# Kernel optimization log

Measured on AMD Instinct MI355X. Metric: run time of the kernel, lower is better.

Reference implementation:

```python
import jax, jax.numpy as jnp
import numpy as np
import math

HIDDEN = 1024

def setup_inputs() -> dict:
    key = jax.random.key(0)
    k1, k2, k3, k4, k5 = jax.random.split(key, 5)
    s = 1.0 / math.sqrt(HIDDEN)
    return {
        "x": jax.random.normal(k1, (4, 2048, HIDDEN), dtype=jnp.float32),
        "W_qkv": jax.random.uniform(k2, (HIDDEN, 3 * HIDDEN), jnp.float32, -s, s),
        "b_qkv": jax.random.uniform(k3, (3 * HIDDEN,), jnp.float32, -s, s),
        "W_out": jax.random.uniform(k4, (HIDDEN, HIDDEN), jnp.float32, -s, s),
        "b_out": jax.random.uniform(k5, (HIDDEN,), jnp.float32, -s, s),
    }

def reference(x, W_qkv, b_qkv, W_out, b_out):
    # fused QKV projection: [b, s, 3h]
    qkv = jnp.einsum("bsh,hd->bsd", x, W_qkv) + b_qkv
    q, k, v = jnp.split(qkv, 3, axis=-1)
    scale = 1.0 / math.sqrt(x.shape[-1])
    scores = jnp.einsum("bqh,bkh->bqk", q, k) * scale  # [b, s, s]
    attn = jax.nn.softmax(scores, axis=-1)
    out = jnp.einsum("bqk,bkh->bqh", attn, v)
    return jnp.einsum("bsh,hd->bsd", out, W_out) + b_out
```

## Files before the change

kernel.cpp:

```cpp
#include <hip/hip_runtime.h>
#include <cstdint>
#include <cstddef>


typedef __bf16 bf16;
typedef __bf16 bf16x8 __attribute__((ext_vector_type(8)));
typedef __bf16 bf16x4 __attribute__((ext_vector_type(4)));
typedef float  f32x4  __attribute__((ext_vector_type(4)));

#define THREADS 512
#define BM 256
#define BN 256
#define UNIT 8192

__device__ __forceinline__ void gload_lds16(const bf16* g, bf16* l) {
  __builtin_amdgcn_global_load_lds(
      (const __attribute__((address_space(1))) unsigned int*)g,
      (__attribute__((address_space(3))) unsigned int*)l, 16, 0, 0);
}

__device__ __forceinline__ void stage_unit(const bf16* g0, long ld, bf16* ldsu, int tid) {
  const int wv = tid >> 6;
  #pragma unroll
  for (int j = 0; j < 2; ++j) {
    const int c = j * 512 + tid;
    const int r = c >> 3;
    const int sg = (c & 7) ^ (r & 7);
    const int cb = j * 512 + (wv << 6);
    gload_lds16(g0 + (long)r * ld + sg * 8, ldsu + (size_t)cb * 8);
  }
}

__device__ __forceinline__ bf16x8 rd_frag(const bf16* unitb, int r, int s) {
  return *(const bf16x8*)(unitb + (size_t)r * 64 + (size_t)((s ^ (r & 7)) * 8));
}

#define GATE(N)  asm volatile("s_waitcnt vmcnt(" #N ")" ::: "memory")
#define LGKM0()  asm volatile("s_waitcnt lgkmcnt(0)" ::: "memory")
#define SBAR()   __builtin_amdgcn_s_barrier()
#define SCHED0() __builtin_amdgcn_sched_barrier(0)

#define PHASE(DB, MH, NH, RA, RB, STAGE_CODE, GATE_CODE)                         \
  {                                                                              \
    if (RA) {                                                                    \
      _Pragma("unroll") for (int mf = 0; mf < 4; ++mf)                           \
        _Pragma("unroll") for (int ks = 0; ks < 2; ++ks)                         \
          aF[mf][ks] = rd_frag(&lds[DB][MH][0], wsm * 64 + mf * 16 + lr, ks * 4 + lh); \
    }                                                                            \
    if (RB) {                                                                    \
      _Pragma("unroll") for (int nf = 0; nf < 2; ++nf)                           \
        _Pragma("unroll") for (int ks = 0; ks < 2; ++ks)                         \
          bF[NH][nf][ks] = rd_frag(&lds[DB][2 + NH][0], wsn * 32 + nf * 16 + lr, ks * 4 + lh); \
    }                                                                            \
    STAGE_CODE;                                                                  \
    SBAR();                                                                      \
    LGKM0();                                                                     \
    SCHED0();                                                                    \
    __builtin_amdgcn_s_setprio(1);                                               \
    _Pragma("unroll") for (int mf = 0; mf < 4; ++mf)                             \
      _Pragma("unroll") for (int nf = 0; nf < 2; ++nf)                           \
        _Pragma("unroll") for (int ks = 0; ks < 2; ++ks)                         \
          acc[(MH)*4 + mf][(NH)*2 + nf] = __builtin_amdgcn_mfma_f32_16x16x32_bf16( \
              aF[mf][ks], bF[NH][nf][ks], acc[(MH)*4 + mf][(NH)*2 + nf], 0, 0, 0); \
    __builtin_amdgcn_s_setprio(0);                                               \
    GATE_CODE;                                                                   \
    SBAR();                                                                      \
    SCHED0();                                                                    \
  }

template <int MODE>
__device__ __forceinline__ void gemm_body(
    const bf16* __restrict__ A, long sAz, int lda,
    const bf16* __restrict__ B, long sBz, int ldb, int K,
    bf16* __restrict__ p0, long sCz, bf16* __restrict__ p1, bf16* __restrict__ p2,
    float* __restrict__ fout, const float* __restrict__ bias, float scale) {
  __shared__ bf16 lds[2][4][UNIT];
  const int tid = threadIdx.x;
  const int wv = tid >> 6, ln = tid & 63;
  const int wsm = wv >> 2, wsn = wv & 3;
  const int lr = ln & 15, lh = ln >> 4;

  const int gx = gridDim.x, gy = gridDim.y;
  const int lin = blockIdx.x + gx * (blockIdx.y + gy * blockIdx.z);
  const int nwg = gx * gy * gridDim.z;
  const int swz = (lin & 7) * (nwg >> 3) + (lin >> 3);
  const int bx = swz % gx;
  const int tq = swz / gx;
  const int by = tq % gy;
  const int z  = tq / gy;

  const int m0 = bx * BM, n0 = by * BN;
  const bf16* Ag = A + (long)z * sAz + (long)m0 * lda;
  const bf16* Bg = B + (long)z * sBz + (long)n0 * ldb;
  const int NITER = K / 128;

  stage_unit(Ag,             lda, &lds[0][0][0], tid);
  stage_unit(Bg,             ldb, &lds[0][2][0], tid);
  stage_unit(Ag + 128 * lda, lda, &lds[0][1][0], tid);
  stage_unit(Bg + 128 * ldb, ldb, &lds[0][3][0], tid);
  stage_unit(Ag + 64,        lda, &lds[1][0][0], tid);
  stage_unit(Bg + 64,        ldb, &lds[1][2][0], tid);
  GATE(8);
  SBAR();
  SCHED0();

  f32x4 acc[8][4];
  #pragma unroll
  for (int i = 0; i < 8; ++i)
    #pragma unroll
    for (int j = 0; j < 4; ++j) acc[i][j] = f32x4{0.f, 0.f, 0.f, 0.f};
  bf16x8 aF[4][2], bF[2][2][2];

  for (int it = 0; it < NITER; ++it) {
    const bool nl = (it + 1 < NITER);
    const long ktA = 2L * it + 1, ktB = 2L * it + 2, ktC = 2L * it + 3;
    PHASE(0, 0, 0, 1, 1,
      { stage_unit(Ag + 128 * lda + ktA * 64, lda, &lds[1][1][0], tid); },
      { GATE(6); });
    PHASE(0, 0, 1, 0, 1,
      { stage_unit(Bg + 128 * ldb + ktA * 64, ldb, &lds[1][3][0], tid); },
      { GATE(10); });
    PHASE(0, 1, 0, 1, 0,
      { if (nl) stage_unit(Ag + ktB * 64, lda, &lds[0][0][0], tid); },
      {});
    PHASE(0, 1, 1, 0, 0,
      { if (nl) stage_unit(Bg + ktB * 64, ldb, &lds[0][2][0], tid); },
      { if (nl) { GATE(8); } else { GATE(4); } });
    PHASE(1, 0, 0, 1, 1,
      { if (nl) stage_unit(Ag + 128 * lda + ktB * 64, lda, &lds[0][1][0], tid); },
      { if (nl) { GATE(6); } else { GATE(0); } });
    PHASE(1, 0, 1, 0, 1,
      { if (nl) stage_unit(Bg + 128 * ldb + ktB * 64, ldb, &lds[0][3][0], tid); },
      { GATE(10); });
    PHASE(1, 1, 0, 1, 0,
      { if (nl) stage_unit(Ag + ktC * 64, lda, &lds[1][0][0], tid); },
      {});
    PHASE(1, 1, 1, 0, 0,
      { if (nl) stage_unit(Bg + ktC * 64, ldb, &lds[1][2][0], tid); },
      { GATE(8); });
  }

  #pragma unroll
  for (int mi = 0; mi < 8; ++mi) {
    #pragma unroll
    for (int ni = 0; ni < 4; ++ni) {
      #pragma unroll
      for (int rg = 0; rg < 4; ++rg) {
        const int gm = m0 + (mi >> 2) * 128 + wsm * 64 + (mi & 3) * 16 + lh * 4 + rg;
        const int gn = n0 + (ni >> 1) * 128 + wsn * 32 + (ni & 1) * 16 + lr;
        float v = acc[mi][ni][rg];
        if constexpr (MODE == 0) {
          v += bias[gn];
          if (gn < 1024)       p0[(size_t)gm * 1024 + gn] = (bf16)v;
          else if (gn < 2048)  p1[(size_t)gm * 1024 + (gn - 1024)] = (bf16)v;
          else                 p2[(size_t)gm * 1024 + (gn - 2048)] = (bf16)v;
        } else if constexpr (MODE == 1) {
          p0[(size_t)z * sCz + (size_t)gm * 2048 + gn] = (bf16)(v * scale);
        } else if constexpr (MODE == 2) {
          p0[(size_t)z * sCz + (size_t)gm * 1024 + gn] = (bf16)v;
        } else {
          fout[(size_t)gm * 1024 + gn] = v + bias[gn];
        }
      }
    }
  }
}

#define GEMM_ARGS const bf16* A, long sAz, int lda, const bf16* B, long sBz, int ldb, \
                  int K, bf16* p0, long sCz, bf16* p1, bf16* p2, float* fout,         \
                  const float* bias, float scale
__global__ __launch_bounds__(THREADS, 2) void gemm_qkv(GEMM_ARGS) {
  gemm_body<0>(A, sAz, lda, B, sBz, ldb, K, p0, sCz, p1, p2, fout, bias, scale);
}
__global__ __launch_bounds__(THREADS, 2) void gemm_sc(GEMM_ARGS) {
  gemm_body<1>(A, sAz, lda, B, sBz, ldb, K, p0, sCz, p1, p2, fout, bias, scale);
}
__global__ __launch_bounds__(THREADS, 2) void gemm_pv(GEMM_ARGS) {
  gemm_body<2>(A, sAz, lda, B, sBz, ldb, K, p0, sCz, p1, p2, fout, bias, scale);
}
__global__ __launch_bounds__(THREADS, 2) void gemm_out(GEMM_ARGS) {
  gemm_body<3>(A, sAz, lda, B, sBz, ldb, K, p0, sCz, p1, p2, fout, bias, scale);
}

__global__ __launch_bounds__(256) void k_f32_to_bf16(const float* __restrict__ in,
                                                     bf16* __restrict__ out, long n) {
  long i = ((long)blockIdx.x * blockDim.x + threadIdx.x) * 4;
  if (i + 3 < n) {
    float4 v = *(const float4*)(in + i);
    bf16x4 o;
    o[0] = (bf16)v.x; o[1] = (bf16)v.y; o[2] = (bf16)v.z; o[3] = (bf16)v.w;
    *(bf16x4*)(out + i) = o;
  }
}

__global__ __launch_bounds__(256) void k_transpose(const float* __restrict__ in,
                                                   bf16* __restrict__ out, int R, int C) {
  __shared__ float t[32][33];
  int c0 = blockIdx.x * 32, r0 = blockIdx.y * 32;
  int tx = threadIdx.x, ty = threadIdx.y;
  #pragma unroll
  for (int dy = 0; dy < 32; dy += 8)
    t[ty + dy][tx] = in[(size_t)(r0 + ty + dy) * C + c0 + tx];
  __syncthreads();
  #pragma unroll
  for (int dy = 0; dy < 32; dy += 8)
    out[(size_t)(c0 + ty + dy) * R + r0 + tx] = (bf16)t[tx][ty + dy];
}

__global__ __launch_bounds__(256) void k_transpose_v(const bf16* __restrict__ in,
                                                     bf16* __restrict__ out) {
  __shared__ bf16 t[32][33];
  const int z = blockIdx.z;
  in  += (size_t)z * 2048 * 1024;
  out += (size_t)z * 1024 * 2048;
  int h0 = blockIdx.x * 32, s0 = blockIdx.y * 32;
  int tx = threadIdx.x, ty = threadIdx.y;
  #pragma unroll
  for (int dy = 0; dy < 32; dy += 8)
    t[ty + dy][tx] = in[(size_t)(s0 + ty + dy) * 1024 + h0 + tx];
  __syncthreads();
  #pragma unroll
  for (int dy = 0; dy < 32; dy += 8)
    out[(size_t)(h0 + ty + dy) * 2048 + s0 + tx] = t[tx][ty + dy];
}

__global__ __launch_bounds__(256) void k_softmax(bf16* __restrict__ S) {
  const int row = blockIdx.x;
  bf16* p = S + (size_t)row * 2048;
  const int tid = threadIdx.x;
  bf16x8 vin = *(const bf16x8*)(p + tid * 8);
  float x[8];
  float mx = -1e30f;
  #pragma unroll
  for (int i = 0; i < 8; ++i) { x[i] = (float)vin[i]; mx = fmaxf(mx, x[i]); }
  #pragma unroll
  for (int off = 32; off; off >>= 1) mx = fmaxf(mx, __shfl_down(mx, off));
  __shared__ float redm[4];
  if ((tid & 63) == 0) redm[tid >> 6] = mx;
  __syncthreads();
  mx = fmaxf(fmaxf(redm[0], redm[1]), fmaxf(redm[2], redm[3]));
  float s = 0.f;
  #pragma unroll
  for (int i = 0; i < 8; ++i) { x[i] = __expf(x[i] - mx); s += x[i]; }
  #pragma unroll
  for (int off = 32; off; off >>= 1) s += __shfl_down(s, off);
  __shared__ float reds[4];
  if ((tid & 63) == 0) reds[tid >> 6] = s;
  __syncthreads();
  s = reds[0] + reds[1] + reds[2] + reds[3];
  float inv = 1.0f / s;
  bf16x8 vo;
  #pragma unroll
  for (int i = 0; i < 8; ++i) vo[i] = (bf16)(x[i] * inv);
  *(bf16x8*)(p + tid * 8) = vo;
}

extern "C" void kernel_launch(void* const* d_in, const int* in_sizes, int n_in,
                              void* d_out, int out_size, void* d_ws, size_t ws_size,
                              hipStream_t stream) {
  const float* x    = (const float*)d_in[0];
  const float* Wqkv = (const float*)d_in[1];
  const float* bqkv = (const float*)d_in[2];
  const float* Wout = (const float*)d_in[3];
  const float* bout = (const float*)d_in[4];
  float* out = (float*)d_out;

  char* w = (char*)d_ws;
  const size_t MB = 1ull << 20;
  bf16* Xb  = (bf16*)(w);
  bf16* WqT = (bf16*)(w + 16 * MB);
  bf16* WoT = (bf16*)(w + 22 * MB);
  bf16* Qb  = (bf16*)(w + 24 * MB);
  bf16* Kb  = (bf16*)(w + 40 * MB);
  bf16* Vb  = (bf16*)(w + 56 * MB);
  bf16* Sb  = (bf16*)(w + 72 * MB);
  bf16* AO  = (bf16*)(w + 104 * MB);
  bf16* VT  = Xb;

  k_f32_to_bf16<<<8192, 256, 0, stream>>>(x, Xb, 8388608L);
  dim3 tb(32, 8);
  k_transpose<<<dim3(96, 32), tb, 0, stream>>>(Wqkv, WqT, 1024, 3072);
  k_transpose<<<dim3(32, 32), tb, 0, stream>>>(Wout, WoT, 1024, 1024);

  gemm_qkv<<<dim3(32, 12), THREADS, 0, stream>>>(
      Xb, 0L, 1024, WqT, 0L, 1024, 1024, Qb, 0L, Kb, Vb, nullptr, bqkv, 1.0f);

  k_transpose_v<<<dim3(32, 64, 4), tb, 0, stream>>>(Vb, VT);

  gemm_sc<<<dim3(8, 8, 4), THREADS, 0, stream>>>(
      Qb, 2048L * 1024, 1024, Kb, 2048L * 1024, 1024, 1024,
      Sb, 2048L * 2048, nullptr, nullptr, nullptr, nullptr, 0.03125f);

  k_softmax<<<8192, 256, 0, stream>>>(Sb);

  gemm_pv<<<dim3(8, 4, 4), THREADS, 0, stream>>>(
      Sb, 2048L * 2048, 2048, VT, 1024L * 2048, 2048, 2048,
      AO, 2048L * 1024, nullptr, nullptr, nullptr, nullptr, 1.0f);

  gemm_out<<<dim3(32, 4), THREADS, 0, stream>>>(
      AO, 0L, 1024, WoT, 0L, 1024, 1024,
      nullptr, 0L, nullptr, nullptr, out, bout, 1.0f);
}
```

Before: 245.7 us.

## Add 256x128 triple-buffered GEMM for QKV, PV and output projections

New measurement: 217.4 us. -11.5%, faster.

```diff
diff --git a/kernel.cpp b/kernel.cpp
--- a/kernel.cpp
+++ b/kernel.cpp
@@ -9,8 +9,6 @@
 typedef float  f32x4  __attribute__((ext_vector_type(4)));
 
 #define THREADS 512
-#define BM 256
-#define BN 256
 #define UNIT 8192
 
 __device__ __forceinline__ void gload_lds16(const bf16* g, bf16* l) {
@@ -39,6 +37,155 @@
 #define LGKM0()  asm volatile("s_waitcnt lgkmcnt(0)" ::: "memory")
 #define SBAR()   __builtin_amdgcn_s_barrier()
 #define SCHED0() __builtin_amdgcn_sched_barrier(0)
+
+#define BM2 256
+#define BN2 128
+#define BK2 64
+#define BUFELS (3*UNIT)
+
+template <int MODE>
+__device__ __forceinline__ void gemm2_body(
+    const bf16* __restrict__ A, long sAz, int lda,
+    const bf16* __restrict__ B, long sBz, int ldb, int K,
+    bf16* __restrict__ p0, long sCz, bf16* __restrict__ p1, bf16* __restrict__ p2,
+    float* __restrict__ fout, const float* __restrict__ bias, float scale) {
+  __shared__ bf16 lds[3 * BUFELS];
+  const int tid = threadIdx.x;
+  const int wv = tid >> 6, ln = tid & 63;
+  const int wr = wv >> 1, wc = wv & 1;
+  const int lr = ln & 15, lh = ln >> 4;
+  const int m0 = blockIdx.x * BM2, n0 = blockIdx.y * BN2;
+  const int z = blockIdx.z;
+  A += (long)z * sAz;
+  B += (long)z * sBz;
+  const bf16* Ag = A + (long)m0 * lda;
+  const bf16* Bg = B + (long)n0 * ldb;
+  const int NT = K / BK2;
+
+  #pragma unroll
+  for (int t = 0; t < 2; ++t) {
+    bf16* bb = lds + t * BUFELS;
+    stage_unit(Ag + t * BK2, lda, bb, tid);
+    stage_unit(Ag + (long)128 * lda + t * BK2, lda, bb + UNIT, tid);
+    stage_unit(Bg + t * BK2, ldb, bb + 2 * UNIT, tid);
+  }
+  GATE(6);
+  SCHED0();
+  SBAR();
+
+  f32x4 acc[4][4];
+  #pragma unroll
+  for (int i = 0; i < 4; ++i)
+    #pragma unroll
+    for (int j = 0; j < 4; ++j)
+      acc[i][j] = f32x4{0.f, 0.f, 0.f, 0.f};
+
+  const int aru = (wr & 1) * 64;
+  const int au  = wr >> 1;
+
+  int buf = 0, nb = 2;
+  for (int t = 0; t < NT; ++t) {
+    const bf16* Au = lds + buf * BUFELS + au * UNIT;
+    const bf16* Bu = lds + buf * BUFELS + 2 * UNIT;
+    bf16* Pn = lds + nb * BUFELS;
+    const bool pf = (t + 2 < NT);
+    bf16x8 aF[2][2], bF[4][2];
+
+    #pragma unroll
+    for (int i = 0; i < 2; ++i)
+      #pragma unroll
+      for (int ks = 0; ks < 2; ++ks)
+        aF[i][ks] = rd_frag(Au, aru + i * 16 + lr, (ks << 2) + lh);
+    #pragma unroll
+    for (int nf = 0; nf < 4; ++nf)
+      #pragma unroll
+      for (int ks = 0; ks < 2; ++ks)
+        bF[nf][ks] = rd_frag(Bu, wc * 64 + nf * 16 + lr, (ks << 2) + lh);
+    if (pf) {
+      stage_unit(Ag + (long)(t + 2) * BK2, lda, Pn, tid);
+      stage_unit(Ag + (long)128 * lda + (long)(t + 2) * BK2, lda, Pn + UNIT, tid);
+    }
+    SBAR();
+    LGKM0();
+    SCHED0();
+    __builtin_amdgcn_s_setprio(1);
+    #pragma unroll
+    for (int i = 0; i < 2; ++i)
+      #pragma unroll
+      for (int nf = 0; nf < 4; ++nf)
+        #pragma unroll
+        for (int ks = 0; ks < 2; ++ks)
+          acc[i][nf] = __builtin_amdgcn_mfma_f32_16x16x32_bf16(aF[i][ks], bF[nf][ks], acc[i][nf], 0, 0, 0);
+    __builtin_amdgcn_s_setprio(0);
+    SBAR();
+
+    #pragma unroll
+    for (int i = 0; i < 2; ++i)
+      #pragma unroll
+      for (int ks = 0; ks < 2; ++ks)
+        aF[i][ks] = rd_frag(Au, aru + 32 + i * 16 + lr, (ks << 2) + lh);
+    if (pf) stage_unit(Bg + (long)(t + 2) * BK2, ldb, Pn + 2 * UNIT, tid);
+    SBAR();
+    LGKM0();
+    SCHED0();
+    __builtin_amdgcn_s_setprio(1);
+    #pragma unroll
+    for (int i = 0; i < 2; ++i)
+      #pragma unroll
+      for (int nf = 0; nf < 4; ++nf)
+        #pragma unroll
+        for (int ks = 0; ks < 2; ++ks)
+          acc[2 + i][nf] = __builtin_amdgcn_mfma_f32_16x16x32_bf16(aF[i][ks], bF[nf][ks], acc[2 + i][nf], 0, 0, 0);
+    __builtin_amdgcn_s_setprio(0);
+    if (t + 1 < NT) {
+      if (pf) { GATE(6); } else { GATE(0); }
+      SCHED0();
+    }
+    SBAR();
+
+    buf = (buf == 2) ? 0 : buf + 1;
+    nb  = (nb == 2) ? 0 : nb + 1;
+  }
+
+  #pragma unroll
+  for (int mf = 0; mf < 4; ++mf) {
+    #pragma unroll
+    for (int nf = 0; nf < 4; ++nf) {
+      #pragma unroll
+      for (int rg = 0; rg < 4; ++rg) {
+        const int gm = m0 + wr * 64 + mf * 16 + lh * 4 + rg;
+        const int gn = n0 + wc * 64 + nf * 16 + lr;
+        float v = acc[mf][nf][rg];
+        if constexpr (MODE == 0) {
+          v += bias[gn];
+          if (gn < 1024)       p0[(size_t)gm * 1024 + gn] = (bf16)v;
+          else if (gn < 2048)  p1[(size_t)gm * 1024 + (gn - 1024)] = (bf16)v;
+          else                 p2[(size_t)gm * 1024 + (gn - 2048)] = (bf16)v;
+        } else if constexpr (MODE == 2) {
+          p0[(size_t)z * sCz + (size_t)gm * 1024 + gn] = (bf16)v;
+        } else {
+          fout[(size_t)gm * 1024 + gn] = v + bias[gn];
+        }
+      }
+    }
+  }
+}
+
+#define GEMM_ARGS const bf16* A, long sAz, int lda, const bf16* B, long sBz, int ldb, \
+                  int K, bf16* p0, long sCz, bf16* p1, bf16* p2, float* fout,         \
+                  const float* bias, float scale
+__global__ __launch_bounds__(THREADS, 2) void gemm_qkv(GEMM_ARGS) {
+  gemm2_body<0>(A, sAz, lda, B, sBz, ldb, K, p0, sCz, p1, p2, fout, bias, scale);
+}
+__global__ __launch_bounds__(THREADS, 2) void gemm_pv(GEMM_ARGS) {
+  gemm2_body<2>(A, sAz, lda, B, sBz, ldb, K, p0, sCz, p1, p2, fout, bias, scale);
+}
+__global__ __launch_bounds__(THREADS, 2) void gemm_out(GEMM_ARGS) {
+  gemm2_body<3>(A, sAz, lda, B, sBz, ldb, K, p0, sCz, p1, p2, fout, bias, scale);
+}
+
+#define BM8 256
+#define BN8 256
 
 #define PHASE(DB, MH, NH, RA, RB, STAGE_CODE, GATE_CODE)                         \
   {                                                                              \
@@ -68,12 +215,10 @@
     SCHED0();                                                                    \
   }
 
-template <int MODE>
-__device__ __forceinline__ void gemm_body(
+__global__ __launch_bounds__(THREADS, 2) void gemm_sc(
     const bf16* __restrict__ A, long sAz, int lda,
     const bf16* __restrict__ B, long sBz, int ldb, int K,
-    bf16* __restrict__ p0, long sCz, bf16* __restrict__ p1, bf16* __restrict__ p2,
-    float* __restrict__ fout, const float* __restrict__ bias, float scale) {
+    bf16* __restrict__ p0, long sCz, float scale) {
   __shared__ bf16 lds[2][4][UNIT];
   const int tid = threadIdx.x;
   const int wv = tid >> 6, ln = tid & 63;
@@ -84,12 +229,12 @@
   const int lin = blockIdx.x + gx * (blockIdx.y + gy * blockIdx.z);
   const int nwg = gx * gy * gridDim.z;
   const int swz = (lin & 7) * (nwg >> 3) + (lin >> 3);
-  const int bx = swz % gx;
-  const int tq = swz / gx;
-  const int by = tq % gy;
-  const int z  = tq / gy;
-
-  const int m0 = bx * BM, n0 = by * BN;
+  const int by = swz % gy;
+  const int t2 = swz / gy;
+  const int bx = t2 % gx;
+  const int z  = t2 / gx;
+
+  const int m0 = bx * BM8, n0 = by * BN8;
   const bf16* Ag = A + (long)z * sAz + (long)m0 * lda;
   const bf16* Bg = B + (long)z * sBz + (long)n0 * ldb;
   const int NITER = K / 128;
@@ -148,38 +293,10 @@
       for (int rg = 0; rg < 4; ++rg) {
         const int gm = m0 + (mi >> 2) * 128 + wsm * 64 + (mi & 3) * 16 + lh * 4 + rg;
         const int gn = n0 + (ni >> 1) * 128 + wsn * 32 + (ni & 1) * 16 + lr;
-        float v = acc[mi][ni][rg];
-        if constexpr (MODE == 0) {
-          v += bias[gn];
-          if (gn < 1024)       p0[(size_t)gm * 1024 + gn] = (bf16)v;
-          else if (gn < 2048)  p1[(size_t)gm * 1024 + (gn - 1024)] = (bf16)v;
-          else                 p2[(size_t)gm * 1024 + (gn - 2048)] = (bf16)v;
-        } else if constexpr (MODE == 1) {
-          p0[(size_t)z * sCz + (size_t)gm * 2048 + gn] = (bf16)(v * scale);
-        } else if constexpr (MODE == 2) {
-          p0[(size_t)z * sCz + (size_t)gm * 1024 + gn] = (bf16)v;
-        } else {
-          fout[(size_t)gm * 1024 + gn] = v + bias[gn];
-        }
+        p0[(size_t)z * sCz + (size_t)gm * 2048 + gn] = (bf16)(acc[mi][ni][rg] * scale);
       }
     }
   }
-}
-
-#define GEMM_ARGS const bf16* A, long sAz, int lda, const bf16* B, long sBz, int ldb, \
-                  int K, bf16* p0, long sCz, bf16* p1, bf16* p2, float* fout,         \
-                  const float* bias, float scale
-__global__ __launch_bounds__(THREADS, 2) void gemm_qkv(GEMM_ARGS) {
-  gemm_body<0>(A, sAz, lda, B, sBz, ldb, K, p0, sCz, p1, p2, fout, bias, scale);
-}
-__global__ __launch_bounds__(THREADS, 2) void gemm_sc(GEMM_ARGS) {
-  gemm_body<1>(A, sAz, lda, B, sBz, ldb, K, p0, sCz, p1, p2, fout, bias, scale);
-}
-__global__ __launch_bounds__(THREADS, 2) void gemm_pv(GEMM_ARGS) {
-  gemm_body<2>(A, sAz, lda, B, sBz, ldb, K, p0, sCz, p1, p2, fout, bias, scale);
-}
-__global__ __launch_bounds__(THREADS, 2) void gemm_out(GEMM_ARGS) {
-  gemm_body<3>(A, sAz, lda, B, sBz, ldb, K, p0, sCz, p1, p2, fout, bias, scale);
 }
 
 __global__ __launch_bounds__(256) void k_f32_to_bf16(const float* __restrict__ in,
@@ -209,18 +326,18 @@
 
 __global__ __launch_bounds__(256) void k_transpose_v(const bf16* __restrict__ in,
                                                      bf16* __restrict__ out) {
-  __shared__ bf16 t[32][33];
+  __shared__ bf16 t[64][65];
   const int z = blockIdx.z;
   in  += (size_t)z * 2048 * 1024;
   out += (size_t)z * 1024 * 2048;
-  int h0 = blockIdx.x * 32, s0 = blockIdx.y * 32;
+  int h0 = blockIdx.x * 64, s0 = blockIdx.y * 64;
   int tx = threadIdx.x, ty = threadIdx.y;
   #pragma unroll
-  for (int dy = 0; dy < 32; dy += 8)
+  for (int dy = 0; dy < 64; dy += 4)
     t[ty + dy][tx] = in[(size_t)(s0 + ty + dy) * 1024 + h0 + tx];
   __syncthreads();
   #pragma unroll
-  for (int dy = 0; dy < 32; dy += 8)
+  for (int dy = 0; dy < 64; dy += 4)
     out[(size_t)(h0 + ty + dy) * 2048 + s0 + tx] = t[tx][ty + dy];
 }
 
@@ -282,22 +399,22 @@
   k_transpose<<<dim3(96, 32), tb, 0, stream>>>(Wqkv, WqT, 1024, 3072);
   k_transpose<<<dim3(32, 32), tb, 0, stream>>>(Wout, WoT, 1024, 1024);
 
-  gemm_qkv<<<dim3(32, 12), THREADS, 0, stream>>>(
+  gemm_qkv<<<dim3(32, 24), THREADS, 0, stream>>>(
       Xb, 0L, 1024, WqT, 0L, 1024, 1024, Qb, 0L, Kb, Vb, nullptr, bqkv, 1.0f);
 
-  k_transpose_v<<<dim3(32, 64, 4), tb, 0, stream>>>(Vb, VT);
+  k_transpose_v<<<dim3(16, 32, 4), dim3(64, 4), 0, stream>>>(Vb, VT);
 
   gemm_sc<<<dim3(8, 8, 4), THREADS, 0, stream>>>(
       Qb, 2048L * 1024, 1024, Kb, 2048L * 1024, 1024, 1024,
-      Sb, 2048L * 2048, nullptr, nullptr, nullptr, nullptr, 0.03125f);
+      Sb, 2048L * 2048, 0.03125f);
 
   k_softmax<<<8192, 256, 0, stream>>>(Sb);
 
-  gemm_pv<<<dim3(8, 4, 4), THREADS, 0, stream>>>(
+  gemm_pv<<<dim3(8, 8, 4), THREADS, 0, stream>>>(
       Sb, 2048L * 2048, 2048, VT, 1024L * 2048, 2048, 2048,
       AO, 2048L * 1024, nullptr, nullptr, nullptr, nullptr, 1.0f);
 
-  gemm_out<<<dim3(32, 4), THREADS, 0, stream>>>(
+  gemm_out<<<dim3(32, 8), THREADS, 0, stream>>>(
       AO, 0L, 1024, WoT, 0L, 1024, 1024,
       nullptr, 0L, nullptr, nullptr, out, bout, 1.0f);
 }
```
